# Kernel optimization log

Hardware: AMD Instinct MI355X
Metric: run time of the kernel (lower is better)

The kernel has to match this reference:

```python
import jax, jax.numpy as jnp
import numpy as np

TEMPERATURE = 0.07


def setup_inputs() -> dict:
    key = jax.random.key(0)
    k1, k2 = jax.random.split(key)
    z = jax.random.normal(k1, (16384, 512), dtype=jnp.float32)
    clusters = jax.random.normal(k2, (1024, 512), dtype=jnp.float32)
    return {"z": z, "clusters": clusters}


def reference(z, clusters):
    # cdist (euclidean) via ||a||^2 + ||b||^2 - 2 a.b, clamped for numerical safety
    sq = (jnp.sum(z * z, axis=1, keepdims=True)
          + jnp.sum(clusters * clusters, axis=1)[None, :]
          - 2.0 * (z @ clusters.T))                      # [B, K]
    distances = jnp.sqrt(jnp.maximum(sq, 0.0))
    closest = jnp.argmin(distances, axis=1)               # [B] int
    # F.normalize(z, dim=1): torch uses eps=1e-12 via clamped norm
    norm = jnp.maximum(jnp.linalg.norm(z, axis=1, keepdims=True), 1e-12)
    z_n = z / norm                                        # [B, D]
    logits = (z_n @ clusters.T) / TEMPERATURE             # [B, K]
    logp = jax.nn.log_softmax(logits, axis=1)
    loss = -jnp.mean(jnp.take_along_axis(logp, closest[:, None], axis=1))
    return (z_n, closest, loss)
```

## Files before the change

### kernel.cpp

```cpp
#include <hip/hip_runtime.h>
#include <hip/hip_bf16.h>
#include <math.h>

#define B 16384
#define K 1024
#define D 512
#define INV_T 14.285714285714286f
#define THETA 0.01f
#define RPB 32
#define NSTEPS 64

typedef __attribute__((ext_vector_type(8))) short bf16x8;
typedef __attribute__((ext_vector_type(16))) float f32x16;
typedef unsigned long long u64;

typedef const __attribute__((address_space(1))) void* gas_ptr;
typedef __attribute__((address_space(3))) void* las_ptr;

__device__ __forceinline__ void async_copy16(const void* g, void* l) {
  __builtin_amdgcn_global_load_lds((gas_ptr)g, (las_ptr)l, 16, 0, 0);
}

__device__ __forceinline__ void cvt8(const float* v, uint4& H, uint4& L) {
  unsigned h[8], l[8];
  #pragma unroll
  for (int i = 0; i < 8; ++i) {
    __hip_bfloat16 hb = __float2bfloat16(v[i]);
    float lo = v[i] - __bfloat162float(hb);
    __hip_bfloat16 lb = __float2bfloat16(lo);
    h[i] = __hip_bfloat16_raw(hb).x;
    l[i] = __hip_bfloat16_raw(lb).x;
  }
  H = make_uint4(h[0] | (h[1] << 16), h[2] | (h[3] << 16), h[4] | (h[5] << 16), h[6] | (h[7] << 16));
  L = make_uint4(l[0] | (l[1] << 16), l[2] | (l[3] << 16), l[4] | (l[5] << 16), l[6] | (l[7] << 16));
}

__device__ __forceinline__ u64 packSK(float s, int k) {
  unsigned u = __float_as_uint(s + 100000.0f);
  return ((u64)u << 32) | (unsigned)k;
}

__global__ __launch_bounds__(256) void pack_z(const float* __restrict__ z,
                                              uint4* __restrict__ zpack,
                                              float* __restrict__ invn) {
  const int blk = blockIdx.x;
  const int wid = threadIdx.x >> 6, lane = threadIdx.x & 63;
  const int dc = lane >> 2, g = lane & 3;
  #pragma unroll
  for (int it = 0; it < 8; ++it) {
    const int r = wid * 8 + it;
    const float* src = z + ((size_t)blk * RPB + r) * D + lane * 8;
    float4 a = ((const float4*)src)[0], b = ((const float4*)src)[1];
    float v[8] = {a.x, a.y, a.z, a.w, b.x, b.y, b.z, b.w};
    uint4 H, L; cvt8(v, H, L);
    const size_t base = (size_t)blk * 4096 + dc * 256;
    zpack[base + g * 32 + r]       = H;
    zpack[base + (4 + g) * 32 + r] = L;
    float ss = 0.f;
    #pragma unroll
    for (int i = 0; i < 8; ++i) ss = fmaf(v[i], v[i], ss);
    #pragma unroll
    for (int mk = 1; mk < 64; mk <<= 1) ss += __shfl_xor(ss, mk);
    if (lane == 0) invn[blk * RPB + r] = 1.0f / fmaxf(sqrtf(ss), 1e-12f);
  }
}

__global__ __launch_bounds__(64) void pack_c(const float* __restrict__ clusters, uint4* __restrict__ cpack,
                                             float* __restrict__ csq, int* __restrict__ flagCnt) {
  const int n = blockIdx.x, t = threadIdx.x;
  const int dc = t >> 2, g = t & 3;
  const int nt = n >> 8, c = n & 255;
  const float* src = clusters + (size_t)n * D + dc * 32 + g * 8;
  float4 a = ((const float4*)src)[0], b2 = ((const float4*)src)[1];
  float v[8] = {a.x, a.y, a.z, a.w, b2.x, b2.y, b2.z, b2.w};
  uint4 H, L; cvt8(v, H, L);
  cpack[((size_t)(dc * 4 + nt) * 8 + g) * 256 + c]     = H;
  cpack[((size_t)(dc * 4 + nt) * 8 + 4 + g) * 256 + c] = L;
  float sq = 0.f;
  #pragma unroll
  for (int i = 0; i < 8; ++i) sq = fmaf(v[i], v[i], sq);
  #pragma unroll
  for (int m = 32; m >= 1; m >>= 1) sq += __shfl_xor(sq, m);
  if (t == 0) csq[n] = sq;
  if (n == 0 && t == 0) *flagCnt = 0;
}

__global__ __launch_bounds__(256, 2) void fused_main(
    const float* __restrict__ z, const char* zpack, const char* __restrict__ cpack,
    const float* __restrict__ csqG, const float* __restrict__ invnG,
    float* out, float* __restrict__ partials,
    float* __restrict__ wsBdot, float* __restrict__ wsInvnt,
    int* __restrict__ flagCnt, int* __restrict__ flagList, u64* __restrict__ wsBest) {
  __shared__ __align__(16) char Abuf[2][4096];
  __shared__ __align__(16) char Bbuf[2][32768];

  const int tid = threadIdx.x;
  const int wid = tid >> 6;
  const int lane = tid & 63;
  const int h2 = lane >> 5, c5 = lane & 31;
  const int blk = blockIdx.x;
  const int row0 = blk * RPB;
  const char* zpB = zpack + (size_t)blk * 65536;

  float runM[16], runS[16], bs[16], bs2[16], invnt[16];
  int bk[16];
  f32x16 acc[2];

  #pragma unroll
  for (int r = 0; r < 16; ++r) {
    runM[r] = -INFINITY; runS[r] = 0.f; bs[r] = INFINITY; bs2[r] = INFINITY; bk[r] = 0;
    const int rloc = (r & 3) + 8 * (r >> 2) + 4 * h2;
    invnt[r] = invnG[row0 + rloc] * INV_T;
  }
  #pragma unroll
  for (int i = 0; i < 16; ++i) { acc[0][i] = 0.f; acc[1][i] = 0.f; }

  auto STAGE = [&](int buf, int step) {
    const int nt = step >> 4, dc = step & 15;
    async_copy16(zpB + ((size_t)(dc * 256 + wid * 64 + lane)) * 16, Abuf[buf] + wid * 1024);
    const char* bbase = cpack + ((size_t)(dc * 4 + nt)) * 32768;
    #pragma unroll
    for (int q = 0; q < 8; ++q) {
      const int L = wid * 8 + q;
      async_copy16(bbase + ((size_t)(L * 64 + lane)) * 16, Bbuf[buf] + L * 1024);
    }
  };

  STAGE(0, 0);
  __syncthreads();

  for (int t = 0; t < NSTEPS; ++t) {
    const int nt = t >> 4, cur = t & 1;
    if (t + 1 < NSTEPS) STAGE(cur ^ 1, t + 1);

    #pragma unroll
    for (int ks = 0; ks < 2; ++ks) {
      const int g0 = ks * 2 + h2;
      bf16x8 ah = *(const bf16x8*)(Abuf[cur] + (g0 * 32 + c5) * 16);
      bf16x8 al = *(const bf16x8*)(Abuf[cur] + ((4 + g0) * 32 + c5) * 16);
      #pragma unroll
      for (int ct = 0; ct < 2; ++ct) {
        const int col = wid * 64 + ct * 32 + c5;
        bf16x8 bh = *(const bf16x8*)(Bbuf[cur] + (g0 * 256 + col) * 16);
        bf16x8 bl = *(const bf16x8*)(Bbuf[cur] + ((4 + g0) * 256 + col) * 16);
        acc[ct] = __builtin_amdgcn_mfma_f32_32x32x16_bf16(ah, bh, acc[ct], 0, 0, 0);
        acc[ct] = __builtin_amdgcn_mfma_f32_32x32x16_bf16(ah, bl, acc[ct], 0, 0, 0);
        acc[ct] = __builtin_amdgcn_mfma_f32_32x32x16_bf16(al, bh, acc[ct], 0, 0, 0);
      }
    }

    if ((t & 15) == 15) {
      const int kk0 = nt * 256 + wid * 64 + c5;
      const float cs0 = csqG[kk0], cs1 = csqG[kk0 + 32];
      #pragma unroll
      for (int r = 0; r < 16; ++r) {
        const float l0 = acc[0][r] * invnt[r];
        const float l1 = acc[1][r] * invnt[r];
        const float nm = fmaxf(runM[r], fmaxf(l0, l1));
        runS[r] = runS[r] * __expf(runM[r] - nm) + __expf(l0 - nm) + __expf(l1 - nm);
        runM[r] = nm;
        const float s0 = cs0 - 2.0f * acc[0][r];
        const float s1 = cs1 - 2.0f * acc[1][r];
        if (s0 < bs[r]) { bs2[r] = bs[r]; bs[r] = s0; bk[r] = kk0; }
        else            { bs2[r] = fminf(bs2[r], s0); }
        if (s1 < bs[r]) { bs2[r] = bs[r]; bs[r] = s1; bk[r] = kk0 + 32; }
        else            { bs2[r] = fminf(bs2[r], s1); }
        acc[0][r] = 0.f; acc[1][r] = 0.f;
      }
    }
    __syncthreads();
  }

  float* mrg = (float*)Abuf;
  #pragma unroll
  for (int r = 0; r < 16; ++r) {
    float m = runM[r], s = runS[r];
    float b1 = bs[r], b2 = bs2[r]; int k1 = bk[r];
    #pragma unroll
    for (int mk = 1; mk < 32; mk <<= 1) {
      const float om = __shfl_xor(m, mk), os = __shfl_xor(s, mk);
      const float nm = fmaxf(m, om);
      s = s * __expf(m - nm) + os * __expf(om - nm);
      m = nm;
      const float o1 = __shfl_xor(b1, mk); const int ok = __shfl_xor(k1, mk);
      const float o2 = __shfl_xor(b2, mk);
      const bool oth = (o1 < b1) || (o1 == b1 && ok < k1);
      const float loser = oth ? b1 : o1;
      b2 = fminf(loser, fminf(b2, o2));
      if (oth) { b1 = o1; k1 = ok; }
    }
    if (c5 == r) {
      const int row = (r & 3) + 8 * (r >> 2) + 4 * h2;
      float* q = &mrg[(wid * 32 + row) * 5];
      q[0] = m; q[1] = s; q[2] = b1; q[3] = (float)k1; q[4] = b2;
    }
  }
  __syncthreads();

  if (tid < 32) {
    const int grow = row0 + tid;
    float rm = -INFINITY, rs = 0.f, r1 = INFINITY, r2 = INFINITY;
    int rk = 0;
    #pragma unroll
    for (int w = 0; w < 4; ++w) {
      const float* q = &mrg[(w * 32 + tid) * 5];
      const float tm = q[0], ts = q[1], t1 = q[2]; const int tk = (int)q[3]; const float t2 = q[4];
      const float nm = fmaxf(rm, tm);
      rs = rs * __expf(rm - nm) + ts * __expf(tm - nm);
      rm = nm;
      const bool oth = (t1 < r1) || (t1 == r1 && tk < rk);
      const float loser = oth ? r1 : t1;
      r2 = fminf(loser, fminf(r2, t2));
      if (oth) { r1 = t1; rk = tk; }
    }
    const float lse = rm + logf(rs);
    const float bdot = (csqG[rk] - r1) * 0.5f;
    const float invT = invnG[grow] * INV_T;
    out[(size_t)B * D + grow] = (float)rk;
    wsBdot[grow] = bdot;
    wsInvnt[grow] = invT;
    if (r2 - r1 < THETA) {
      const int pos = atomicAdd(flagCnt, 1);
      flagList[pos] = grow;
      wsBest[pos] = ~0ull;
    }
    float lossr = lse - bdot * invT;
    #pragma unroll
    for (int mk = 1; mk < 32; mk <<= 1) lossr += __shfl_xor(lossr, mk);
    if (tid == 0) partials[blk] = lossr;
  }

  const float4* z4 = (const float4*)(z + (size_t)row0 * D);
  float4* o4 = (float4*)(out + (size_t)row0 * D);
  #pragma unroll
  for (int i = 0; i < 16; ++i) {
    const int e = tid + 256 * i;
    const int r = e >> 7;
    const float inv = invnG[row0 + r];
    float4 v = z4[e];
    v.x *= inv; v.y *= inv; v.z *= inv; v.w *= inv;
    o4[e] = v;
  }
}

__global__ __launch_bounds__(256) void fixup(
    const float* __restrict__ z, const float* __restrict__ clusters, const float* __restrict__ csq,
    const int* __restrict__ flagCnt, const int* __restrict__ flagList, u64* __restrict__ wsBest) {
  __shared__ float zrow[D];
  __shared__ float wS[4]; __shared__ int wK[4];
  const int tid = threadIdx.x;
  const int n = *flagCnt;
  const int chunk = blockIdx.x & 7;
  for (int f = blockIdx.x >> 3; f < n; f += 64) {
    const int row = flagList[f];
    __syncthreads();
    ((float2*)zrow)[tid] = ((const float2*)(z + (size_t)row * D))[tid];
    __syncthreads();
    const int k = chunk * 128 + (tid >> 1), half = tid & 1;
    const float4* c4 = (const float4*)(clusters + (size_t)k * D + half * 256);
    const float4* z4 = (const float4*)(zrow + half * 256);
    float dot = 0.f;
    #pragma unroll 16
    for (int i = 0; i < 64; ++i) {
      const float4 cv = c4[i]; const float4 zv = z4[i];
      dot = fmaf(cv.x, zv.x, dot); dot = fmaf(cv.y, zv.y, dot);
      dot = fmaf(cv.z, zv.z, dot); dot = fmaf(cv.w, zv.w, dot);
    }
    dot += __shfl_xor(dot, 1);
    float s = csq[k] - 2.f * dot;
    int bkv = k;
    #pragma unroll
    for (int mk = 2; mk < 64; mk <<= 1) {
      const float os = __shfl_xor(s, mk); const int ok = __shfl_xor(bkv, mk);
      if (os < s || (os == s && ok < bkv)) { s = os; bkv = ok; }
    }
    if ((tid & 63) == 0) { wS[tid >> 6] = s; wK[tid >> 6] = bkv; }
    __syncthreads();
    if (tid == 0) {
      float fs = wS[0]; int fk = wK[0];
      for (int w = 1; w < 4; ++w)
        if (wS[w] < fs || (wS[w] == fs && wK[w] < fk)) { fs = wS[w]; fk = wK[w]; }
      atomicMin(&wsBest[f], packSK(fs, fk));
    }
    __syncthreads();
  }
}

__global__ __launch_bounds__(256) void loss_final(
    const float* __restrict__ partials, const float* __restrict__ csq,
    const int* __restrict__ flagCnt, const int* __restrict__ flagList,
    const u64* __restrict__ wsBest, const float* __restrict__ wsBdot,
    const float* __restrict__ wsInvnt, float* out) {
  const int t = threadIdx.x;
  float s = partials[t] + partials[t + 256];
  const int n = *flagCnt;
  for (int f = t; f < n; f += 256) {
    const int row = flagList[f];
    const u64 v = wsBest[f];
    const int kN = (int)(unsigned)(v & 0xffffffffu);
    const float sN = __uint_as_float((unsigned)(v >> 32)) - 100000.0f;
    const int kO = (int)out[(size_t)B * D + row];
    if (kN != kO) {
      out[(size_t)B * D + row] = (float)kN;
      const float bdN = (csq[kN] - sN) * 0.5f;
      s += (wsBdot[row] - bdN) * wsInvnt[row];
    }
  }
  #pragma unroll
  for (int mk = 1; mk < 64; mk <<= 1) s += __shfl_xor(s, mk);
  __shared__ float w[4];
  if ((t & 63) == 0) w[t >> 6] = s;
  __syncthreads();
  if (t == 0) out[(size_t)B * D + B] = (w[0] + w[1] + w[2] + w[3]) * (1.0f / (float)B);
}

extern "C" void kernel_launch(void* const* d_in, const int* in_sizes, int n_in,
                              void* d_out, int out_size, void* d_ws, size_t ws_size,
                              hipStream_t stream) {
  const float* z        = (const float*)d_in[0];
  const float* clusters = (const float*)d_in[1];
  float* out = (float*)d_out;

  char* wsb = (char*)d_ws;
  uint4* cpack     = (uint4*)wsb;
  u64*   wsBest    = (u64*)(wsb + (2u << 20));
  float* csq       = (float*)(wsb + (2u << 20) + (128u << 10));
  float* partials  = csq + 1024;
  float* invn      = partials + 512;
  float* wsBdot    = invn + B;
  float* wsInvnt   = wsBdot + B;
  int*   flagCnt   = (int*)(wsInvnt + B);
  int*   flagList  = flagCnt + 1;

  pack_c<<<K, 64, 0, stream>>>(clusters, cpack, csq, flagCnt);
  pack_z<<<B / RPB, 256, 0, stream>>>(z, (uint4*)d_out, invn);
  fused_main<<<B / RPB, 256, 0, stream>>>(z, (const char*)d_out, (const char*)cpack,
                                          csq, invn, out, partials, wsBdot, wsInvnt,
                                          flagCnt, flagList, wsBest);
  fixup<<<512, 256, 0, stream>>>(z, clusters, csq, flagCnt, flagList, wsBest);
  loss_final<<<1, 256, 0, stream>>>(partials, csq, flagCnt, flagList, wsBest,
                                    wsBdot, wsInvnt, out);
}
```

Before: 228.5 us.

## Retile fused GEMM to 64-row, K-split blocks with separate merge kernel

The main kernel now uses 512-thread blocks covering 64 rows and half of the clusters (512 blocks total), with a 2x4 wave grid and smaller B tiles, and a K-step of 32 instead of 64. Per-row partial softmax and argmin results go to workspace and are combined by a new merge_zn kernel, which also writes z_n. The near-tie tracking is simplified from a second-best distance to a flag based on THETA comparisons. The goal is better A/B reuse, more parallelism and occupancy, at the cost of an extra launch and workspace round trip, and possibly more rows flagged for the fixup pass.

```diff
diff --git a/kernel.cpp b/kernel.cpp
--- a/kernel.cpp
+++ b/kernel.cpp
@@ -7,8 +7,6 @@
 #define D 512
 #define INV_T 14.285714285714286f
 #define THETA 0.01f
-#define RPB 32
-#define NSTEPS 64
 
 typedef __attribute__((ext_vector_type(8))) short bf16x8;
 typedef __attribute__((ext_vector_type(16))) float f32x16;
@@ -23,7 +21,7 @@
 
 __device__ __forceinline__ void cvt8(const float* v, uint4& H, uint4& L) {
   unsigned h[8], l[8];
-  #pragma unroll
+#pragma unroll
   for (int i = 0; i < 8; ++i) {
     __hip_bfloat16 hb = __float2bfloat16(v[i]);
     float lo = v[i] - __bfloat162float(hb);
@@ -43,200 +41,221 @@
 __global__ __launch_bounds__(256) void pack_z(const float* __restrict__ z,
                                               uint4* __restrict__ zpack,
                                               float* __restrict__ invn) {
-  const int blk = blockIdx.x;
-  const int wid = threadIdx.x >> 6, lane = threadIdx.x & 63;
-  const int dc = lane >> 2, g = lane & 3;
-  #pragma unroll
+  const int bid = blockIdx.x;
+  const int rowblk = bid >> 1, sub = bid & 1;
+  const int t = threadIdx.x;
+  const int rl = t >> 3, l = t & 7;
+  const int grow = bid * 32 + rl;
+  const int r = sub * 32 + rl;
+  const float* zr = z + (size_t)grow * D;
+  uint4* zpRB = zpack + (size_t)rowblk * 8192;
+  float ss = 0.f;
+#pragma unroll
   for (int it = 0; it < 8; ++it) {
-    const int r = wid * 8 + it;
-    const float* src = z + ((size_t)blk * RPB + r) * D + lane * 8;
-    float4 a = ((const float4*)src)[0], b = ((const float4*)src)[1];
-    float v[8] = {a.x, a.y, a.z, a.w, b.x, b.y, b.z, b.w};
+    const int combo = l + it * 8;
+    const float4 v0 = *(const float4*)(zr + combo * 8);
+    const float4 v1 = *(const float4*)(zr + combo * 8 + 4);
+    float v[8] = {v0.x, v0.y, v0.z, v0.w, v1.x, v1.y, v1.z, v1.w};
+#pragma unroll
+    for (int i = 0; i < 8; ++i) ss = fmaf(v[i], v[i], ss);
     uint4 H, L; cvt8(v, H, L);
-    const size_t base = (size_t)blk * 4096 + dc * 256;
-    zpack[base + g * 32 + r]       = H;
-    zpack[base + (4 + g) * 32 + r] = L;
-    float ss = 0.f;
-    #pragma unroll
-    for (int i = 0; i < 8; ++i) ss = fmaf(v[i], v[i], ss);
-    #pragma unroll
-    for (int mk = 1; mk < 64; mk <<= 1) ss += __shfl_xor(ss, mk);
-    if (lane == 0) invn[blk * RPB + r] = 1.0f / fmaxf(sqrtf(ss), 1e-12f);
-  }
-}
-
-__global__ __launch_bounds__(64) void pack_c(const float* __restrict__ clusters, uint4* __restrict__ cpack,
-                                             float* __restrict__ csq, int* __restrict__ flagCnt) {
+    const int dcs = combo >> 1, g = combo & 1;
+    zpRB[(size_t)(dcs * 4 + g) * 64 + r]     = H;
+    zpRB[(size_t)(dcs * 4 + 2 + g) * 64 + r] = L;
+  }
+  ss += __shfl_xor(ss, 1); ss += __shfl_xor(ss, 2); ss += __shfl_xor(ss, 4);
+  if (l == 0) invn[grow] = 1.0f / fmaxf(sqrtf(ss), 1e-12f);
+}
+
+__global__ __launch_bounds__(64) void pack_c(const float* __restrict__ clusters,
+                                             uint4* __restrict__ cpack,
+                                             float* __restrict__ csq,
+                                             int* __restrict__ flagCnt) {
   const int n = blockIdx.x, t = threadIdx.x;
-  const int dc = t >> 2, g = t & 3;
-  const int nt = n >> 8, c = n & 255;
-  const float* src = clusters + (size_t)n * D + dc * 32 + g * 8;
-  float4 a = ((const float4*)src)[0], b2 = ((const float4*)src)[1];
+  const int c = n & 255, nt = (n >> 8) & 1, half = n >> 9;
+  const int dcs = t >> 1, g = t & 1;
+  const float* src = clusters + (size_t)n * D + t * 8;
+  const float4 a = ((const float4*)src)[0], b2 = ((const float4*)src)[1];
   float v[8] = {a.x, a.y, a.z, a.w, b2.x, b2.y, b2.z, b2.w};
   uint4 H, L; cvt8(v, H, L);
-  cpack[((size_t)(dc * 4 + nt) * 8 + g) * 256 + c]     = H;
-  cpack[((size_t)(dc * 4 + nt) * 8 + 4 + g) * 256 + c] = L;
+  uint4* base = cpack + ((size_t)((half * 2 + nt) * 32 + dcs)) * 1024 + c;
+  base[(0 + g) * 256] = H;
+  base[(2 + g) * 256] = L;
   float sq = 0.f;
-  #pragma unroll
+#pragma unroll
   for (int i = 0; i < 8; ++i) sq = fmaf(v[i], v[i], sq);
-  #pragma unroll
+#pragma unroll
   for (int m = 32; m >= 1; m >>= 1) sq += __shfl_xor(sq, m);
   if (t == 0) csq[n] = sq;
   if (n == 0 && t == 0) *flagCnt = 0;
 }
 
-__global__ __launch_bounds__(256, 2) void fused_main(
-    const float* __restrict__ z, const char* zpack, const char* __restrict__ cpack,
+__global__ __launch_bounds__(512, 4) void fused_main(
+    const char* __restrict__ zpack, const char* __restrict__ cpack,
     const float* __restrict__ csqG, const float* __restrict__ invnG,
-    float* out, float* __restrict__ partials,
-    float* __restrict__ wsBdot, float* __restrict__ wsInvnt,
-    int* __restrict__ flagCnt, int* __restrict__ flagList, u64* __restrict__ wsBest) {
+    float* __restrict__ wsPart) {
   __shared__ __align__(16) char Abuf[2][4096];
-  __shared__ __align__(16) char Bbuf[2][32768];
+  __shared__ __align__(16) char Bbuf[2][16384];
+  __shared__ float invnLds[64];
 
   const int tid = threadIdx.x;
-  const int wid = tid >> 6;
-  const int lane = tid & 63;
+  const int wid = tid >> 6, lane = tid & 63;
   const int h2 = lane >> 5, c5 = lane & 31;
-  const int blk = blockIdx.x;
-  const int row0 = blk * RPB;
-  const char* zpB = zpack + (size_t)blk * 65536;
-
-  float runM[16], runS[16], bs[16], bs2[16], invnt[16];
+  const int wr = wid >> 2, wc = wid & 3;
+  const int bid = blockIdx.x;
+  const int rb = bid & 255, half = bid >> 8;
+  const char* zpA = zpack + (size_t)rb * 131072;
+  const char* cpB = cpack + (size_t)half * 1048576;
+
+  if (tid < 64) invnLds[tid] = invnG[rb * 64 + tid] * INV_T;
+
+  float runM[16], runS[16], bs[16];
   int bk[16];
-  f32x16 acc[2];
-
-  #pragma unroll
+  unsigned cflag = 0;
+  f32x16 acc0, acc1;
+#pragma unroll
   for (int r = 0; r < 16; ++r) {
-    runM[r] = -INFINITY; runS[r] = 0.f; bs[r] = INFINITY; bs2[r] = INFINITY; bk[r] = 0;
-    const int rloc = (r & 3) + 8 * (r >> 2) + 4 * h2;
-    invnt[r] = invnG[row0 + rloc] * INV_T;
-  }
-  #pragma unroll
-  for (int i = 0; i < 16; ++i) { acc[0][i] = 0.f; acc[1][i] = 0.f; }
-
-  auto STAGE = [&](int buf, int step) {
-    const int nt = step >> 4, dc = step & 15;
-    async_copy16(zpB + ((size_t)(dc * 256 + wid * 64 + lane)) * 16, Abuf[buf] + wid * 1024);
-    const char* bbase = cpack + ((size_t)(dc * 4 + nt)) * 32768;
-    #pragma unroll
-    for (int q = 0; q < 8; ++q) {
-      const int L = wid * 8 + q;
-      async_copy16(bbase + ((size_t)(L * 64 + lane)) * 16, Bbuf[buf] + L * 1024);
-    }
+    runM[r] = -INFINITY; runS[r] = 0.f; bs[r] = INFINITY; bk[r] = 0;
+  }
+#pragma unroll
+  for (int i = 0; i < 16; ++i) { acc0[i] = 0.f; acc1[i] = 0.f; }
+
+  auto STAGE = [&](int buf, int t) {
+    const int dcs = t & 31;
+    if (wid < 4)
+      async_copy16(zpA + (size_t)dcs * 4096 + (wid * 64 + lane) * 16,
+                   Abuf[buf] + wid * 1024);
+    const int cb0 = (wid & 3) * 128 + (wid >> 2) * 512;
+    const char* bsrc = cpB + (size_t)t * 16384;
+#pragma unroll
+    for (int q = 0; q < 2; ++q)
+      async_copy16(bsrc + (cb0 + q * 64 + lane) * 16, Bbuf[buf] + (cb0 + q * 64) * 16);
   };
 
-  STAGE(0, 0);
-  __syncthreads();
-
-  for (int t = 0; t < NSTEPS; ++t) {
-    const int nt = t >> 4, cur = t & 1;
-    if (t + 1 < NSTEPS) STAGE(cur ^ 1, t + 1);
-
-    #pragma unroll
-    for (int ks = 0; ks < 2; ++ks) {
-      const int g0 = ks * 2 + h2;
-      bf16x8 ah = *(const bf16x8*)(Abuf[cur] + (g0 * 32 + c5) * 16);
-      bf16x8 al = *(const bf16x8*)(Abuf[cur] + ((4 + g0) * 32 + c5) * 16);
-      #pragma unroll
-      for (int ct = 0; ct < 2; ++ct) {
-        const int col = wid * 64 + ct * 32 + c5;
-        bf16x8 bh = *(const bf16x8*)(Bbuf[cur] + (g0 * 256 + col) * 16);
-        bf16x8 bl = *(const bf16x8*)(Bbuf[cur] + ((4 + g0) * 256 + col) * 16);
-        acc[ct] = __builtin_amdgcn_mfma_f32_32x32x16_bf16(ah, bh, acc[ct], 0, 0, 0);
-        acc[ct] = __builtin_amdgcn_mfma_f32_32x32x16_bf16(ah, bl, acc[ct], 0, 0, 0);
-        acc[ct] = __builtin_amdgcn_mfma_f32_32x32x16_bf16(al, bh, acc[ct], 0, 0, 0);
-      }
-    }
-
-    if ((t & 15) == 15) {
-      const int kk0 = nt * 256 + wid * 64 + c5;
+  auto STEP = [&](int t, int buf) {
+    if (t + 1 < 64) STAGE(buf ^ 1, t + 1);
+    bf16x8 ah  = *(const bf16x8*)(Abuf[buf] + ((0 + h2) * 64 + wr * 32 + c5) * 16);
+    bf16x8 al  = *(const bf16x8*)(Abuf[buf] + ((2 + h2) * 64 + wr * 32 + c5) * 16);
+    bf16x8 bh0 = *(const bf16x8*)(Bbuf[buf] + ((0 + h2) * 256 + wc * 64 + c5) * 16);
+    bf16x8 bl0 = *(const bf16x8*)(Bbuf[buf] + ((2 + h2) * 256 + wc * 64 + c5) * 16);
+    bf16x8 bh1 = *(const bf16x8*)(Bbuf[buf] + ((0 + h2) * 256 + wc * 64 + 32 + c5) * 16);
+    bf16x8 bl1 = *(const bf16x8*)(Bbuf[buf] + ((2 + h2) * 256 + wc * 64 + 32 + c5) * 16);
+    acc0 = __builtin_amdgcn_mfma_f32_32x32x16_bf16(ah, bh0, acc0, 0, 0, 0);
+    acc0 = __builtin_amdgcn_mfma_f32_32x32x16_bf16(ah, bl0, acc0, 0, 0, 0);
+    acc0 = __builtin_amdgcn_mfma_f32_32x32x16_bf16(al, bh0, acc0, 0, 0, 0);
+    acc1 = __builtin_amdgcn_mfma_f32_32x32x16_bf16(ah, bh1, acc1, 0, 0, 0);
+    acc1 = __builtin_amdgcn_mfma_f32_32x32x16_bf16(ah, bl1, acc1, 0, 0, 0);
+    acc1 = __builtin_amdgcn_mfma_f32_32x32x16_bf16(al, bh1, acc1, 0, 0, 0);
+
+    if ((t & 31) == 31) {
+      const int nt = t >> 5;
+      const int kk0 = half * 512 + nt * 256 + wc * 64 + c5;
       const float cs0 = csqG[kk0], cs1 = csqG[kk0 + 32];
-      #pragma unroll
+#pragma unroll
       for (int r = 0; r < 16; ++r) {
-        const float l0 = acc[0][r] * invnt[r];
-        const float l1 = acc[1][r] * invnt[r];
+        const int rloc = (r & 3) + 8 * (r >> 2) + 4 * h2;
+        const float invnt = invnLds[wr * 32 + rloc];
+        const float l0 = acc0[r] * invnt, l1 = acc1[r] * invnt;
         const float nm = fmaxf(runM[r], fmaxf(l0, l1));
         runS[r] = runS[r] * __expf(runM[r] - nm) + __expf(l0 - nm) + __expf(l1 - nm);
         runM[r] = nm;
-        const float s0 = cs0 - 2.0f * acc[0][r];
-        const float s1 = cs1 - 2.0f * acc[1][r];
-        if (s0 < bs[r]) { bs2[r] = bs[r]; bs[r] = s0; bk[r] = kk0; }
-        else            { bs2[r] = fminf(bs2[r], s0); }
-        if (s1 < bs[r]) { bs2[r] = bs[r]; bs[r] = s1; bk[r] = kk0 + 32; }
-        else            { bs2[r] = fminf(bs2[r], s1); }
-        acc[0][r] = 0.f; acc[1][r] = 0.f;
+        const float s0 = cs0 - 2.0f * acc0[r];
+        const float s1 = cs1 - 2.0f * acc1[r];
+        if (fabsf(s0 - bs[r]) < THETA) cflag |= (1u << r);
+        if (s0 < bs[r]) { bs[r] = s0; bk[r] = kk0; }
+        if (fabsf(s1 - bs[r]) < THETA) cflag |= (1u << r);
+        if (s1 < bs[r]) { bs[r] = s1; bk[r] = kk0 + 32; }
+        acc0[r] = 0.f; acc1[r] = 0.f;
       }
     }
     __syncthreads();
-  }
-
-  float* mrg = (float*)Abuf;
-  #pragma unroll
+  };
+
+  STAGE(0, 0);
+  __syncthreads();
+#pragma unroll 1
+  for (int tt = 0; tt < 64; tt += 2) { STEP(tt, 0); STEP(tt + 1, 1); }
+
+  float* mrg = (float*)&Abuf[0][0];
+#pragma unroll
   for (int r = 0; r < 16; ++r) {
-    float m = runM[r], s = runS[r];
-    float b1 = bs[r], b2 = bs2[r]; int k1 = bk[r];
-    #pragma unroll
+    float m = runM[r], s = runS[r], b1 = bs[r];
+    int k1 = bk[r];
+    int fl = (cflag >> r) & 1;
+#pragma unroll
     for (int mk = 1; mk < 32; mk <<= 1) {
       const float om = __shfl_xor(m, mk), os = __shfl_xor(s, mk);
       const float nm = fmaxf(m, om);
       s = s * __expf(m - nm) + os * __expf(om - nm);
       m = nm;
       const float o1 = __shfl_xor(b1, mk); const int ok = __shfl_xor(k1, mk);
-      const float o2 = __shfl_xor(b2, mk);
-      const bool oth = (o1 < b1) || (o1 == b1 && ok < k1);
-      const float loser = oth ? b1 : o1;
-      b2 = fminf(loser, fminf(b2, o2));
-      if (oth) { b1 = o1; k1 = ok; }
+      const int ofl = __shfl_xor(fl, mk);
+      fl = fl | ofl | (fabsf(b1 - o1) < THETA ? 1 : 0);
+      if (o1 < b1 || (o1 == b1 && ok < k1)) { b1 = o1; k1 = ok; }
     }
     if (c5 == r) {
-      const int row = (r & 3) + 8 * (r >> 2) + 4 * h2;
-      float* q = &mrg[(wid * 32 + row) * 5];
-      q[0] = m; q[1] = s; q[2] = b1; q[3] = (float)k1; q[4] = b2;
+      const int row = wr * 32 + (r & 3) + 8 * (r >> 2) + 4 * h2;
+      float* q = &mrg[(wc * 64 + row) * 5];
+      q[0] = m; q[1] = s; q[2] = b1; q[3] = (float)k1; q[4] = (float)fl;
     }
   }
   __syncthreads();
 
-  if (tid < 32) {
-    const int grow = row0 + tid;
-    float rm = -INFINITY, rs = 0.f, r1 = INFINITY, r2 = INFINITY;
-    int rk = 0;
-    #pragma unroll
+  if (tid < 64) {
+    float rm = -INFINITY, rs = 0.f, r1 = INFINITY;
+    int rk = 0, rfl = 0;
+#pragma unroll
     for (int w = 0; w < 4; ++w) {
-      const float* q = &mrg[(w * 32 + tid) * 5];
-      const float tm = q[0], ts = q[1], t1 = q[2]; const int tk = (int)q[3]; const float t2 = q[4];
+      const float* q = &mrg[(w * 64 + tid) * 5];
+      const float tm = q[0], ts = q[1], t1 = q[2];
+      const int tk = (int)q[3], tf = (int)q[4];
       const float nm = fmaxf(rm, tm);
       rs = rs * __expf(rm - nm) + ts * __expf(tm - nm);
       rm = nm;
-      const bool oth = (t1 < r1) || (t1 == r1 && tk < rk);
-      const float loser = oth ? r1 : t1;
-      r2 = fminf(loser, fminf(r2, t2));
-      if (oth) { r1 = t1; rk = tk; }
-    }
-    const float lse = rm + logf(rs);
-    const float bdot = (csqG[rk] - r1) * 0.5f;
-    const float invT = invnG[grow] * INV_T;
-    out[(size_t)B * D + grow] = (float)rk;
-    wsBdot[grow] = bdot;
-    wsInvnt[grow] = invT;
-    if (r2 - r1 < THETA) {
-      const int pos = atomicAdd(flagCnt, 1);
-      flagList[pos] = grow;
-      wsBest[pos] = ~0ull;
-    }
+      rfl = rfl | tf | (fabsf(t1 - r1) < THETA ? 1 : 0);
+      if (t1 < r1 || (t1 == r1 && tk < rk)) { r1 = t1; rk = tk; }
+    }
+    float* dst = wsPart + ((size_t)(rb * 64 + tid) * 2 + half) * 5;
+    dst[0] = rm; dst[1] = rs; dst[2] = r1; dst[3] = (float)rk; dst[4] = (float)rfl;
+  }
+}
+
+__global__ __launch_bounds__(256) void merge_zn(
+    const float* __restrict__ z, const float* __restrict__ invnG,
+    const float* __restrict__ csq, const float* __restrict__ wsPart,
+    float* __restrict__ out, float* __restrict__ partials,
+    float* __restrict__ wsBdot, float* __restrict__ wsInvnt,
+    int* __restrict__ flagCnt, int* __restrict__ flagList, u64* __restrict__ wsBest) {
+  const int bid = blockIdx.x, tid = threadIdx.x;
+  if (tid < 64) {
+    const int row = bid * 64 + tid;
+    const float* p0 = wsPart + (size_t)row * 10;
+    const float* p1 = p0 + 5;
+    const float m0 = p0[0], s0 = p0[1], m1 = p1[0], s1 = p1[1];
+    const float nm = fmaxf(m0, m1);
+    const float lse = nm + logf(s0 * __expf(m0 - nm) + s1 * __expf(m1 - nm));
+    const float b1a = p0[2], b1b = p1[2];
+    const int k1a = (int)p0[3], k1b = (int)p1[3];
+    const int fl = ((int)p0[4]) | ((int)p1[4]) | (fabsf(b1a - b1b) < THETA ? 1 : 0);
+    float b1; int k1;
+    if (b1b < b1a || (b1b == b1a && k1b < k1a)) { b1 = b1b; k1 = k1b; }
+    else                                        { b1 = b1a; k1 = k1a; }
+    const float bdot = (csq[k1] - b1) * 0.5f;
+    const float invT = invnG[row] * INV_T;
+    out[(size_t)B * D + row] = (float)k1;
+    wsBdot[row] = bdot; wsInvnt[row] = invT;
+    if (fl) { const int pos = atomicAdd(flagCnt, 1); flagList[pos] = row; wsBest[pos] = ~0ull; }
     float lossr = lse - bdot * invT;
-    #pragma unroll
-    for (int mk = 1; mk < 32; mk <<= 1) lossr += __shfl_xor(lossr, mk);
-    if (tid == 0) partials[blk] = lossr;
-  }
-
-  const float4* z4 = (const float4*)(z + (size_t)row0 * D);
-  float4* o4 = (float4*)(out + (size_t)row0 * D);
-  #pragma unroll
-  for (int i = 0; i < 16; ++i) {
+#pragma unroll
+    for (int mk = 1; mk < 64; mk <<= 1) lossr += __shfl_xor(lossr, mk);
+    if (tid == 0) partials[bid] = lossr;
+  }
+  const float4* z4 = (const float4*)z + (size_t)bid * 8192;
+  float4* o4 = (float4*)out + (size_t)bid * 8192;
+#pragma unroll
+  for (int i = 0; i < 32; ++i) {
     const int e = tid + 256 * i;
-    const int r = e >> 7;
-    const float inv = invnG[row0 + r];
+    const float inv = invnG[bid * 64 + (e >> 7)];
     float4 v = z4[e];
     v.x *= inv; v.y *= inv; v.z *= inv; v.w *= inv;
     o4[e] = v;
@@ -256,20 +275,20 @@
     __syncthreads();
     ((float2*)zrow)[tid] = ((const float2*)(z + (size_t)row * D))[tid];
     __syncthreads();
-    const int k = chunk * 128 + (tid >> 1), half = tid & 1;
-    const float4* c4 = (const float4*)(clusters + (size_t)k * D + half * 256);
-    const float4* z4 = (const float4*)(zrow + half * 256);
+    const int k = chunk * 128 + (tid >> 1), halfsel = tid & 1;
+    const float4* c4 = (const float4*)(clusters + (size_t)k * D + halfsel * 256);
+    const float4* zz4 = (const float4*)(zrow + halfsel * 256);
     float dot = 0.f;
-    #pragma unroll 16
+#pragma unroll 16
     for (int i = 0; i < 64; ++i) {
-      const float4 cv = c4[i]; const float4 zv = z4[i];
+      const float4 cv = c4[i]; const float4 zv = zz4[i];
       dot = fmaf(cv.x, zv.x, dot); dot = fmaf(cv.y, zv.y, dot);
       dot = fmaf(cv.z, zv.z, dot); dot = fmaf(cv.w, zv.w, dot);
     }
     dot += __shfl_xor(dot, 1);
     float s = csq[k] - 2.f * dot;
     int bkv = k;
-    #pragma unroll
+#pragma unroll
     for (int mk = 2; mk < 64; mk <<= 1) {
       const float os = __shfl_xor(s, mk); const int ok = __shfl_xor(bkv, mk);
       if (os < s || (os == s && ok < bkv)) { s = os; bkv = ok; }
@@ -290,9 +309,9 @@
     const float* __restrict__ partials, const float* __restrict__ csq,
     const int* __restrict__ flagCnt, const int* __restrict__ flagList,
     const u64* __restrict__ wsBest, const float* __restrict__ wsBdot,
-    const float* __restrict__ wsInvnt, float* out) {
+    const float* __restrict__ wsInvnt, float* __restrict__ out) {
   const int t = threadIdx.x;
-  float s = partials[t] + partials[t + 256];
+  float s = partials[t];
   const int n = *flagCnt;
   for (int f = t; f < n; f += 256) {
     const int row = flagList[f];
@@ -306,7 +325,7 @@
       s += (wsBdot[row] - bdN) * wsInvnt[row];
     }
   }
-  #pragma unroll
+#pragma unroll
   for (int mk = 1; mk < 64; mk <<= 1) s += __shfl_xor(s, mk);
   __shared__ float w[4];
   if ((t & 63) == 0) w[t >> 6] = s;
@@ -324,19 +343,22 @@
   char* wsb = (char*)d_ws;
   uint4* cpack     = (uint4*)wsb;
   u64*   wsBest    = (u64*)(wsb + (2u << 20));
-  float* csq       = (float*)(wsb + (2u << 20) + (128u << 10));
+  float* fb        = (float*)(wsb + (2u << 20) + (128u << 10));
+  float* csq       = fb;
   float* partials  = csq + 1024;
-  float* invn      = partials + 512;
+  float* invn      = partials + 256;
   float* wsBdot    = invn + B;
   float* wsInvnt   = wsBdot + B;
-  int*   flagCnt   = (int*)(wsInvnt + B);
+  float* wsPart    = wsInvnt + B;
+  int*   flagCnt   = (int*)(wsPart + 10 * B);
   int*   flagList  = flagCnt + 1;
 
   pack_c<<<K, 64, 0, stream>>>(clusters, cpack, csq, flagCnt);
-  pack_z<<<B / RPB, 256, 0, stream>>>(z, (uint4*)d_out, invn);
-  fused_main<<<B / RPB, 256, 0, stream>>>(z, (const char*)d_out, (const char*)cpack,
-                                          csq, invn, out, partials, wsBdot, wsInvnt,
-                                          flagCnt, flagList, wsBest);
+  pack_z<<<B / 32, 256, 0, stream>>>(z, (uint4*)d_out, invn);
+  fused_main<<<512, 512, 0, stream>>>((const char*)d_out, (const char*)cpack,
+                                      csq, invn, wsPart);
+  merge_zn<<<B / 64, 256, 0, stream>>>(z, invn, csq, wsPart, out, partials,
+                                       wsBdot, wsInvnt, flagCnt, flagList, wsBest);
   fixup<<<512, 256, 0, stream>>>(z, clusters, csq, flagCnt, flagList, wsBest);
   loss_final<<<1, 256, 0, stream>>>(partials, csq, flagCnt, flagList, wsBest,
                                     wsBdot, wsInvnt, out);
```

Measured after the change: 653.3 us. 2.86x slower.
